# Optimization experiments

Measured on AMD Instinct MI355X. Metric: run time of the kernel, lower is better.

The kernel has to match this reference:

```python
import jax, jax.numpy as jnp
import numpy as np

T, B = 10, 512
N_ALL, N_AGENTS = 23, 22
N_FEAT = 4
X_DIM = 4
Z_EACH = 4
Z_DIM = N_ALL * Z_EACH  # 92
RNN_H = 64
NH = 8
E = N_ALL * (N_ALL - 1)  # 506

# edge list equivalent of the dense one-hot rel_rec / rel_send matrices
_off = np.ones((N_ALL, N_ALL)) - np.eye(N_ALL)
_recv_np, _send_np = np.where(_off)
RECV = jnp.asarray(_recv_np)  # rel_rec one-hot rows -> receiver node ids
SEND = jnp.asarray(_send_np)  # rel_send one-hot rows -> sender node ids
_et = np.zeros((E, 2), np.float32)
_et[np.arange(0, E, N_ALL - 1)[1:-1], 0] = 1.0
_et[-(N_ALL - 1):, 1] = 1.0
EDGE_TYPE = jnp.asarray(_et)
_nt = np.zeros((N_ALL, 2), np.float32)
_nt[:-1, 0] = 1.0
_nt[-1, 1] = 1.0
NODE_TYPE = jnp.asarray(_nt)


def _bn(x, g, b):
    # BatchNorm1d in training mode over flattened (B*M, C), biased variance
    B_, M, C = x.shape
    xf = x.reshape(B_ * M, C)
    mu = xf.mean(0)
    var = jnp.var(xf, axis=0)
    return ((xf - mu) * jax.lax.rsqrt(var + 1e-5) * g + b).reshape(B_, M, C)


def _mlp(x, W1, b1, W2, b2, g, bt):
    h = jax.nn.elu(jnp.einsum('bmi,hi->bmh', x, W1) + b1)
    h = jax.nn.elu(jnp.einsum('bmi,hi->bmh', h, W2) + b2)
    return _bn(h, g, bt)


def _kld(me, se, mp_, sp):
    return 0.5 * jnp.sum(2.0 * jnp.log(sp / se) + (se ** 2 + (me - mp_) ** 2) / sp ** 2 - 1.0)


def _gru_cell(Wih, Whh, bih, bhh, x, h):
    gi = x @ Wih.T + bih
    gh = h @ Whh.T + bhh
    ir, iz, inn = jnp.split(gi, 3, -1)
    hr, hz, hn = jnp.split(gh, 3, -1)
    r = jax.nn.sigmoid(ir + hr)
    z = jax.nn.sigmoid(iz + hz)
    n = jnp.tanh(inn + r * hn)
    return (1.0 - z) * n + z * h


_gru = jax.vmap(_gru_cell)  # over agents


def _forward(states, eps, mlp1_W1, mlp1_b1, mlp1_W2, mlp1_b2, mlp1_g, mlp1_beta,
             mlp2_W1, mlp2_b1, mlp2_W2, mlp2_b2, mlp2_g, mlp2_beta,
             mlp3_W1, mlp3_b1, mlp3_W2, mlp3_b2, mlp3_g, mlp3_beta,
             enc_mean_W, enc_mean_b, enc_std_W, enc_std_b,
             prior_mean_W, prior_mean_b, prior_std_W, prior_std_b,
             dec_mean_W, dec_mean_b, dec_std_W, dec_std_b,
             gru_Wih, gru_Whh, gru_bih, gru_bhh):
    Bsz = states.shape[2]
    y = states[:T, 0].reshape(T, Bsz, N_ALL, N_FEAT)        # y_t
    x1 = states[1:T + 1, 0].reshape(T, Bsz, N_ALL, N_FEAT)  # x_{t+1}
    P1 = (mlp1_W1, mlp1_b1, mlp1_W2, mlp1_b2, mlp1_g, mlp1_beta)
    P2 = (mlp2_W1, mlp2_b1, mlp2_W2, mlp2_b2, mlp2_g, mlp2_beta)
    P3 = (mlp3_W1, mlp3_b1, mlp3_W2, mlp3_b2, mlp3_g, mlp3_beta)

    def gnn(x, p):
        x = _mlp(x, *(a[p] for a in P1))
        # node2edge: gather senders/receivers instead of one-hot matmul
        e = jnp.concatenate([x[:, SEND], x[:, RECV],
                             jnp.broadcast_to(EDGE_TYPE, (Bsz, E, 2))], -1)
        e = _mlp(e, *(a[p] for a in P2))
        # edge2node: scatter-add into receiver nodes (rel_rec.T @ e)
        inc = jnp.zeros((Bsz, N_ALL, NH), x.dtype).at[:, RECV].add(e)
        inc = jnp.concatenate([inc, jnp.broadcast_to(NODE_TYPE, (Bsz, N_ALL, 2))], -1) / N_ALL
        return _mlp(inc, *(a[p] for a in P3))

    def step(carry, xs):
        h, Lkl = carry
        y_t, x_t, eps_t = xs
        micro = jnp.transpose(h, (1, 0, 2)).reshape(Bsz, -1)  # (B, nA*H)
        pri = jnp.concatenate([gnn(y_t, 0).reshape(Bsz, -1), micro], 1)
        enc = jnp.concatenate([gnn(x_t, 1).reshape(Bsz, -1), micro], 1)
        pm = pri @ prior_mean_W.T + prior_mean_b
        ps = jax.nn.softplus(pri @ prior_std_W.T + prior_std_b)
        em = enc @ enc_mean_W.T + enc_mean_b
        es = jax.nn.softplus(enc @ enc_std_W.T + enc_std_b)
        z = em + es * eps_t  # reparameterized sample_gauss
        Lkl = Lkl + _kld(em, es, pm, ps)
        z_ = z.reshape(Bsz, N_ALL, Z_EACH)
        dg = gnn(z_, 2).reshape(Bsz, -1)
        dm = dg @ dec_mean_W.T + dec_mean_b
        ds = jax.nn.softplus(dg @ dec_std_W.T + dec_std_b)
        # per-agent GRU update: input = [x_t agent feats, z slice]
        gin = jnp.transpose(
            jnp.concatenate([x_t[:, :N_AGENTS, :X_DIM], z_[:, :N_AGENTS]], -1), (1, 0, 2))
        h = _gru(gru_Wih, gru_Whh, gru_bih, gru_bhh, gin, h)
        return (h, Lkl), (dm, ds)

    h0 = jnp.zeros((N_AGENTS, Bsz, RNN_H), states.dtype)
    (_, Lkl), (dms, dss) = jax.lax.scan(step, (h0, jnp.zeros((), states.dtype)), (y, x1, eps))
    return dms, dss, Lkl


def setup_inputs() -> dict:
    key = jax.random.key(0)
    ks = iter(jax.random.split(key, 64))

    def rn(shape, s=0.1):
        return jax.random.normal(next(ks), shape, jnp.float32) * s

    d = {}
    d['states'] = rn((T + 1, 1, B, N_ALL * N_FEAT), 1.0)
    d['eps'] = rn((T, B, Z_DIM), 1.0)
    for i, nin in ((1, N_FEAT), (2, 2 * NH + 2), (3, NH + 2)):
        d['mlp%d_W1' % i] = rn((3, NH, nin), 0.3)
        d['mlp%d_b1' % i] = jnp.full((3, NH), 0.1, jnp.float32)
        d['mlp%d_W2' % i] = rn((3, NH, NH), 0.3)
        d['mlp%d_b2' % i] = jnp.full((3, NH), 0.1, jnp.float32)
        d['mlp%d_g' % i] = jnp.ones((3, NH), jnp.float32)
        d['mlp%d_beta' % i] = jnp.zeros((3, NH), jnp.float32)
    IN_H = NH * N_ALL + RNN_H * N_AGENTS  # 1592
    for nm in ('enc_mean', 'enc_std', 'prior_mean', 'prior_std'):
        d[nm + '_W'] = rn((Z_DIM, IN_H), 0.02)
        d[nm + '_b'] = jnp.zeros((Z_DIM,), jnp.float32)
    OUT_DEC = NH * N_ALL  # 184
    for nm in ('dec_mean', 'dec_std'):
        d[nm + '_W'] = rn((X_DIM * N_AGENTS, OUT_DEC), 0.05)
        d[nm + '_b'] = jnp.zeros((X_DIM * N_AGENTS,), jnp.float32)
    d['gru_Wih'] = rn((N_AGENTS, 3 * RNN_H, X_DIM + Z_EACH), 0.2)
    d['gru_Whh'] = rn((N_AGENTS, 3 * RNN_H, RNN_H), 0.1)
    d['gru_bih'] = jnp.zeros((N_AGENTS, 3 * RNN_H), jnp.float32)
    d['gru_bhh'] = jnp.zeros((N_AGENTS, 3 * RNN_H), jnp.float32)
    return d


def reference(states, eps, mlp1_W1, mlp1_b1, mlp1_W2, mlp1_b2, mlp1_g, mlp1_beta,
              mlp2_W1, mlp2_b1, mlp2_W2, mlp2_b2, mlp2_g, mlp2_beta,
              mlp3_W1, mlp3_b1, mlp3_W2, mlp3_b2, mlp3_g, mlp3_beta,
              enc_mean_W, enc_mean_b, enc_std_W, enc_std_b,
              prior_mean_W, prior_mean_b, prior_std_W, prior_std_b,
              dec_mean_W, dec_mean_b, dec_std_W, dec_std_b,
              gru_Wih, gru_Whh, gru_bih, gru_bhh):
    return _forward(states, eps, mlp1_W1, mlp1_b1, mlp1_W2, mlp1_b2, mlp1_g, mlp1_beta,
                    mlp2_W1, mlp2_b1, mlp2_W2, mlp2_b2, mlp2_g, mlp2_beta,
                    mlp3_W1, mlp3_b1, mlp3_W2, mlp3_b2, mlp3_g, mlp3_beta,
                    enc_mean_W, enc_mean_b, enc_std_W, enc_std_b,
                    prior_mean_W, prior_mean_b, prior_std_W, prior_std_b,
                    dec_mean_W, dec_mean_b, dec_std_W, dec_std_b,
                    gru_Wih, gru_Whh, gru_bih, gru_bhh)
```

## Files before the change

### kernel.cpp

```cpp
#include <hip/hip_runtime.h>
#include <math.h>


__device__ __forceinline__ float elu_(float x){ return x>0.f ? x : __expf(x)-1.f; }
__device__ __forceinline__ float sp_(float x){ return fmaxf(x,0.f)+log1pf(__expf(-fabsf(x))); }
__device__ __forceinline__ float sig_(float x){ return 1.f/(1.f+__expf(-x)); }
__device__ __forceinline__ float wsum_(float v){
  #pragma unroll
  for (int o=32;o;o>>=1) v += __shfl_down(v,o,64);
  return v;
}

__device__ __forceinline__ void reduce_bn_(const float* __restrict__ part, int n,
    float invN, const float* __restrict__ gam, const float* __restrict__ bet,
    float* sc, float* sh, float* tmp)
{
  int tid = threadIdx.x;
  int c = tid & 15, i0 = tid >> 4;
  float s = 0.f;
  for (int i = i0; i < n; i += 16) s += part[i*16 + c];
  tmp[i0*16 + c] = s;
  __syncthreads();
  if (tid < 16){
    float v = 0.f;
    #pragma unroll
    for (int i=0;i<16;i++) v += tmp[i*16 + tid];
    tmp[tid] = v;
  }
  __syncthreads();
  if (tid < 8){
    float m = tmp[tid]*invN;
    float var = tmp[8+tid]*invN - m*m;
    float rs = rsqrtf(var + 1e-5f);
    float s2 = rs*gam[tid];
    sc[tid] = s2; sh[tid] = bet[tid] - m*s2;
  }
  __syncthreads();
}

__device__ __forceinline__ void block_stats_(const float h[8], float* __restrict__ part,
                                             float red[][16])
{
  int wid = threadIdx.x >> 6, lane = threadIdx.x & 63;
  #pragma unroll
  for (int j=0;j<8;j++){
    float a = wsum_(h[j]);
    float b = wsum_(h[j]*h[j]);
    if (lane==0){ red[wid][j]=a; red[wid][8+j]=b; }
  }
  __syncthreads();
  if (threadIdx.x < 16)
    part[threadIdx.x] = red[0][threadIdx.x]+red[1][threadIdx.x]
                       +red[2][threadIdx.x]+red[3][threadIdx.x];
}


__device__ __forceinline__ void dev_heads(
    float* smem, int idx, int t,
    const float* __restrict__ gy, const float* __restrict__ gx,
    const float* __restrict__ scsh3, const float* __restrict__ h,
    const float* __restrict__ Wpm, const float* __restrict__ Wps,
    const float* __restrict__ Wem, const float* __restrict__ Wes,
    float* __restrict__ rawp)
{
  int bt = idx & 7, head = (idx>>3)&3, kz = idx>>5;
  const float* W  = (head==0)?Wpm:(head==1)?Wps:(head==2)?Wem:Wes;
  const float* gsel = (head<2)?gy:gx;
  int sel = (head<2) ? t : 10+t;
  float* s3 = smem;
  float (*As)[68]  = (float(*)[68])(smem+16);
  float (*Ws)[100] = (float(*)[100])(smem+1104);
  int tid = threadIdx.x;
  if (tid < 16) s3[tid] = scsh3[sel*16 + tid];
  int b0 = bt*64;
  int kbeg = kz*228;
  int kend = kbeg+228; if (kend > 1592) kend = 1592;
  int tb = tid & 15, tj = tid >> 4;
  float acc[4][6];
  #pragma unroll
  for (int u=0;u<4;u++)
    #pragma unroll
    for (int vv=0;vv<6;vv++) acc[u][vv]=0.f;
  __syncthreads();
  for (int k0=kbeg; k0<kend; k0+=16){
    #pragma unroll
    for (int l=0;l<4;l++){
      int lin = tid + 256*l;
      int kk = lin & 15, bl = lin >> 4;
      int i = k0 + kk;
      float v = 0.f;
      if (i < kend){
        int bb = b0 + bl;
        if (i < 184){ int c = i&7; v = gsel[bb*184 + i]*s3[c] + s3[8+c]; }
        else { int i2 = i - 184; v = h[(size_t)(i2>>6)*32768 + bb*64 + (i2&63)]; }
      }
      As[kk][bl] = v;
    }
    #pragma unroll
    for (int l=0;l<6;l++){
      int lin = tid + 256*l;
      int kk = lin & 15, jl = lin >> 4;
      int i = k0 + kk;
      float v = 0.f;
      if (i < kend && jl < 92) v = W[jl*1592 + i];
      Ws[kk][jl] = v;
    }
    __syncthreads();
    #pragma unroll
    for (int kk=0;kk<16;kk++){
      float4 a4 = *(const float4*)&As[kk][tb*4];
      float av[4] = {a4.x,a4.y,a4.z,a4.w};
      float2 w01 = *(const float2*)&Ws[kk][tj*6];
      float2 w23 = *(const float2*)&Ws[kk][tj*6+2];
      float2 w45 = *(const float2*)&Ws[kk][tj*6+4];
      float wv[6] = {w01.x,w01.y,w23.x,w23.y,w45.x,w45.y};
      #pragma unroll
      for (int u=0;u<4;u++)
        #pragma unroll
        for (int vv=0;vv<6;vv++) acc[u][vv] += av[u]*wv[vv];
    }
    __syncthreads();
  }
  float* dst = rawp + (size_t)kz*188416 + (size_t)head*47104;
  #pragma unroll
  for (int u=0;u<4;u++){
    int bb = b0 + tb*4 + u;
    #pragma unroll
    for (int vv=0;vv<6;vv++){
      int j = tj*6 + vv;
      if (j < 92) dst[bb*92 + j] = acc[u][vv];
    }
  }
}

__device__ __forceinline__ void dev_edges_z(
    float* smem, int b,
    const float* __restrict__ rawp_prev, const float* __restrict__ eps_t,
    const float* __restrict__ bpm, const float* __restrict__ bps,
    const float* __restrict__ bem, const float* __restrict__ bes,
    const float* __restrict__ zp1,
    const float* __restrict__ nW1, const float* __restrict__ nb1,
    const float* __restrict__ nW2, const float* __restrict__ nb2,
    const float* __restrict__ g1, const float* __restrict__ bt1,
    const float* __restrict__ eW1, const float* __restrict__ eb1,
    const float* __restrict__ eW2, const float* __restrict__ eb2,
    float* __restrict__ zna, float* __restrict__ zp2, float* __restrict__ lklp_t)
{
  int tid = threadIdx.x;
  float* tmp   = smem;
  float* sc1   = smem+256;
  float* sh1   = smem+264;
  float* xnode = smem+272;
  float* accs  = smem+480;
  float* redsq = smem+688;
  float* zrow  = smem+720;
  float* redk  = smem+812;
  float* le    = smem+816;
  {
    int c = tid & 15, i0 = tid >> 4;
    float s = 0.f;
    for (int i=i0;i<368;i+=16) s += zp1[i*16+c];
    tmp[i0*16+c] = s;
    __syncthreads();
    if (tid<16){
      float v=0.f;
      #pragma unroll
      for (int i=0;i<16;i++) v += tmp[i*16+tid];
      tmp[tid]=v;
    }
    __syncthreads();
    if (tid<8){
      float m = tmp[tid]*(1.f/11776.f);
      float var = tmp[8+tid]*(1.f/11776.f) - m*m;
      float rs = rsqrtf(var+1e-5f);
      float s2 = rs*g1[tid];
      sc1[tid]=s2; sh1[tid]=bt1[tid]-m*s2;
    }
  }
  float kld = 0.f;
  if (tid < 92){
    int j = tid;
    float pm=bpm[j], ps=bps[j], em=bem[j], es=bes[j];
    const float* q = rawp_prev + (size_t)b*92 + j;
    #pragma unroll
    for (int kz=0;kz<7;kz++){
      const float* qq = q + (size_t)kz*188416;
      pm += qq[0]; ps += qq[47104]; em += qq[94208]; es += qq[141312];
    }
    ps = sp_(ps); es = sp_(es);
    float z = em + es*eps_t[(size_t)b*92 + j];
    zrow[j] = z;
    float d = em - pm;
    kld = 0.5f*(2.f*logf(ps/es) + (es*es + d*d)/(ps*ps) - 1.f);
  }
  float kv = wsum_(kld);
  if ((tid&63)==0) redk[tid>>6] = kv;
  __syncthreads();
  if (tid==0) lklp_t[b] = redk[0]+redk[1]+redk[2]+redk[3];
  if (tid < 23){
    float z0=zrow[tid*4], z1=zrow[tid*4+1], z2=zrow[tid*4+2], z3=zrow[tid*4+3];
    float h1[8];
    #pragma unroll
    for (int j=0;j<8;j++)
      h1[j] = elu_(nb1[j] + nW1[j*4]*z0 + nW1[j*4+1]*z1 + nW1[j*4+2]*z2 + nW1[j*4+3]*z3);
    #pragma unroll
    for (int j=0;j<8;j++){
      float a = nb2[j];
      #pragma unroll
      for (int k=0;k<8;k++) a += nW2[j*8+k]*h1[k];
      xnode[tid*9+j] = elu_(a)*sc1[j] + sh1[j];
    }
  }
  __syncthreads();
  float sq[8]={0,0,0,0,0,0,0,0};
  for (int e=tid; e<506; e+=256){
    int r=e/22, jj=e-r*22;
    int s=jj+(jj>=r?1:0);
    float et0=(jj==0 && r>=1 && r<=21)?1.f:0.f;
    float et1=(r==22)?1.f:0.f;
    float h1[8];
    #pragma unroll
    for (int j=0;j<8;j++){
      const float* w=eW1+j*18;
      float a=eb1[j]+w[16]*et0+w[17]*et1;
      #pragma unroll
      for (int k=0;k<8;k++) a+=w[k]*xnode[s*9+k];
      #pragma unroll
      for (int k=0;k<8;k++) a+=w[8+k]*xnode[r*9+k];
      h1[j]=elu_(a);
    }
    #pragma unroll
    for (int j=0;j<8;j++){
      float a=eb2[j];
      #pragma unroll
      for (int k=0;k<8;k++) a+=eW2[j*8+k]*h1[k];
      float h2=elu_(a);
      le[e*9+j]=h2;
      sq[j]+=h2*h2;
    }
  }
  int wid=tid>>6, lane=tid&63;
  #pragma unroll
  for (int j=0;j<8;j++){
    float v=wsum_(sq[j]);
    if (lane==0) redsq[wid*8+j]=v;
  }
  __syncthreads();
  if (tid<184){
    int r=tid>>3, c=tid&7;
    const float* lp = le + r*198 + c;
    float s=0.f;
    #pragma unroll
    for (int jj=0;jj<22;jj++) s+=lp[jj*9];
    accs[r*9+c]=s;
    zna[(size_t)b*184+tid]=s;
  }
  __syncthreads();
  if (tid<16){
    int c=tid&7;
    float s=0.f;
    if (tid<8){
      #pragma unroll
      for (int r=0;r<23;r++) s+=accs[r*9+c];
    } else {
      #pragma unroll
      for (int w=0;w<4;w++) s+=redsq[w*8+c];
    }
    zp2[(size_t)b*16+tid]=s;
  }
}

__device__ __forceinline__ void dev_node3(
    float* smem, int bi, int g, int p,
    const float* __restrict__ nodeacc, const float* __restrict__ p2,
    const float* __restrict__ g2b, const float* __restrict__ bt2b,
    const float* __restrict__ W3b, const float* __restrict__ b3b,
    const float* __restrict__ W4b, const float* __restrict__ b4b,
    float* __restrict__ out, float* __restrict__ p3)
{
  float* tmp = smem; float* sc2 = smem+256; float* sh2 = smem+264;
  float (*red)[16] = (float(*)[16])(smem+272);
  reduce_bn_(p2 + (size_t)g*8192, 512, 1.f/259072.f, g2b+p*8, bt2b+p*8, sc2, sh2, tmp);
  int row = bi*256 + threadIdx.x;
  int b = row/23, r = row - b*23;
  const float inv23 = 1.f/23.f;
  const float* na = nodeacc + ((size_t)g*512 + b)*184 + r*8;
  float xk[8];
  #pragma unroll
  for (int k=0;k<8;k++) xk[k] = (na[k]*sc2[k] + 22.f*sh2[k]) * inv23;
  float nt0 = (r<22)?inv23:0.f, nt1 = (r==22)?inv23:0.f;
  const float* W3 = W3b + p*80; const float* b3 = b3b + p*8;
  const float* W4 = W4b + p*64; const float* b4 = b4b + p*8;
  float h1b[8], o[8];
  #pragma unroll
  for (int j=0;j<8;j++){
    const float* w = W3 + j*10;
    float a = b3[j] + w[8]*nt0 + w[9]*nt1;
    #pragma unroll
    for (int k=0;k<8;k++) a += w[k]*xk[k];
    h1b[j] = elu_(a);
  }
  #pragma unroll
  for (int j=0;j<8;j++){
    float a = b4[j];
    #pragma unroll
    for (int k=0;k<8;k++) a += W4[j*8+k]*h1b[k];
    o[j] = elu_(a);
    out[((size_t)g*11776 + row)*8 + j] = o[j];
  }
  block_stats_(o, p3 + ((size_t)g*46 + bi)*16, red);
}

__device__ __forceinline__ void dev_dec(
    float* smem, int bi,
    const float* __restrict__ zg3, const float* __restrict__ p3,
    const float* __restrict__ gam, const float* __restrict__ bet,
    const float* __restrict__ Wm, const float* __restrict__ Bm,
    const float* __restrict__ Wsd, const float* __restrict__ Bsd,
    float* __restrict__ odm, float* __restrict__ ods)
{
  int tid = threadIdx.x;
  float* dtmp = smem; float* dsc = smem + 256; float* dsh = smem + 264;
  reduce_bn_(p3, 46, 1.f/11776.f, gam, bet, dsc, dsh, dtmp);
  float4 s0 = {dsc[0],dsc[1],dsc[2],dsc[3]};
  float4 s1 = {dsc[4],dsc[5],dsc[6],dsc[7]};
  float4 t0 = {dsh[0],dsh[1],dsh[2],dsh[3]};
  float4 t1 = {dsh[4],dsh[5],dsh[6],dsh[7]};
  int idx = bi*256 + tid;
  int hd = idx / 45056; int rem = idx - hd*45056;
  int b = rem / 88, j = rem - b*88;
  const float* W = hd ? Wsd : Wm;
  const float4* a4 = (const float4*)(zg3 + (size_t)b*184);
  const float4* w4 = (const float4*)(W + (size_t)j*184);
  float accv = hd ? Bsd[j] : Bm[j];
  #pragma unroll 2
  for (int i4=0;i4<46;i4++){
    float4 x = a4[i4]; float4 w = w4[i4];
    float4 sc = (i4&1)? s1 : s0; float4 sh = (i4&1)? t1 : t0;
    accv += w.x*(x.x*sc.x+sh.x) + w.y*(x.y*sc.y+sh.y)
          + w.z*(x.z*sc.z+sh.z) + w.w*(x.w*sc.w+sh.w);
  }
  if (hd) ods[(size_t)b*88+j] = sp_(accv);
  else    odm[(size_t)b*88+j] = accv;
}

__device__ __forceinline__ void dev_gru_z(
    float* smem, int idx,
    float* __restrict__ h, const float* __restrict__ x_t,
    const float* __restrict__ rawp_cur, const float* __restrict__ eps_t,
    const float* __restrict__ bem, const float* __restrict__ bes,
    const float* __restrict__ nW1, const float* __restrict__ nb1,
    const float* __restrict__ nW2, const float* __restrict__ nb2,
    float* __restrict__ zp1,
    const float* __restrict__ Wih, const float* __restrict__ Whh,
    const float* __restrict__ bih, const float* __restrict__ bhh)
{
  int tid = threadIdx.x;
  float* WhT  = smem;
  float* hs   = smem + 12352;
  float* gins = smem + 14656;
  int a = idx >> 4, yb = idx & 15;
  int b0 = yb*32;
  int c = tid & 63, sq = tid >> 6;
  const float* Wg = Whh + (size_t)a*12288;
  for (int e = tid; e < 12288; e += 256) WhT[(e&63)*193 + (e>>6)] = Wg[e];
  const float* hp_g = h + (size_t)a*32768 + (size_t)b0*64;
  for (int e = tid; e < 2048; e += 256) hs[(e&63)*36 + (e>>6)] = hp_g[e];
  { int s = tid >> 3, k = tid & 7;
    float v;
    if (k < 4) v = x_t[(size_t)(b0+s)*92 + a*4 + k];
    else {
      int j = a*4 + (k-4);
      float em=bem[j], es=bes[j];
      const float* q = rawp_cur + (size_t)(b0+s)*92 + j;
      #pragma unroll
      for (int kz=0;kz<7;kz++){
        const float* qq = q + (size_t)kz*188416;
        em += qq[94208]; es += qq[141312];
      }
      es = sp_(es);
      v = em + es*eps_t[(size_t)(b0+s)*92 + j];
    }
    gins[k*36 + s] = v; }
  float wi0[8], wi1[8], wi2[8];
  const float* Wig = Wih + (size_t)a*1536;
  #pragma unroll
  for (int k=0;k<8;k++){
    wi0[k] = Wig[c*8+k]; wi1[k] = Wig[(64+c)*8+k]; wi2[k] = Wig[(128+c)*8+k];
  }
  float bi0 = bih[a*192+c], bi1 = bih[a*192+64+c], bi2 = bih[a*192+128+c];
  float bh0 = bhh[a*192+c], bh1 = bhh[a*192+64+c], bh2 = bhh[a*192+128+c];
  __syncthreads();
  {
    float h2s[8];
    if (tid < 32){
      float z0=gins[4*36+tid], z1=gins[5*36+tid], z2=gins[6*36+tid], z3=gins[7*36+tid];
      float h1s[8];
      #pragma unroll
      for (int j=0;j<8;j++)
        h1s[j] = elu_(nb1[j] + nW1[j*4]*z0 + nW1[j*4+1]*z1 + nW1[j*4+2]*z2 + nW1[j*4+3]*z3);
      #pragma unroll
      for (int j=0;j<8;j++){
        float av = nb2[j];
        #pragma unroll
        for (int k=0;k<8;k++) av += nW2[j*8+k]*h1s[k];
        h2s[j] = elu_(av);
      }
    } else {
      #pragma unroll
      for (int j=0;j<8;j++) h2s[j] = 0.f;
    }
    float* dst = zp1 + (size_t)(a*16+yb)*16;
    #pragma unroll
    for (int j=0;j<8;j++){
      float s1 = wsum_(h2s[j]);
      float s2 = wsum_(h2s[j]*h2s[j]);
      if (tid==0){ dst[j]=s1; dst[8+j]=s2; }
    }
  }
  #pragma unroll
  for (int ps=0; ps<2; ps++){
    int s0 = ps*16 + sq*4;
    float q0[4], q1[4], q2[4];
    #pragma unroll
    for (int i=0;i<4;i++){ q0[i]=bh0; q1[i]=bh1; q2[i]=bh2; }
    for (int k=0;k<64;k++){
      float w0 = WhT[k*193 + c];
      float w1 = WhT[k*193 + 64 + c];
      float w2 = WhT[k*193 + 128 + c];
      float4 hv = *(const float4*)&hs[k*36 + s0];
      float hvv[4] = {hv.x,hv.y,hv.z,hv.w};
      #pragma unroll
      for (int i=0;i<4;i++){ q0[i]+=w0*hvv[i]; q1[i]+=w1*hvv[i]; q2[i]+=w2*hvv[i]; }
    }
    float g0[4], g1[4], g2[4];
    #pragma unroll
    for (int i=0;i<4;i++){ g0[i]=bi0; g1[i]=bi1; g2[i]=bi2; }
    #pragma unroll
    for (int k=0;k<8;k++){
      float4 gv = *(const float4*)&gins[k*36 + s0];
      float gvv[4] = {gv.x,gv.y,gv.z,gv.w};
      #pragma unroll
      for (int i=0;i<4;i++){ g0[i]+=wi0[k]*gvv[i]; g1[i]+=wi1[k]*gvv[i]; g2[i]+=wi2[k]*gvv[i]; }
    }
    float4 hp = *(const float4*)&hs[c*36 + s0];
    float hpv[4] = {hp.x,hp.y,hp.z,hp.w};
    #pragma unroll
    for (int i=0;i<4;i++){
      float rg = sig_(g0[i]+q0[i]);
      float zg = sig_(g1[i]+q1[i]);
      float ng = tanhf(g2[i] + rg*q2[i]);
      h[(size_t)a*32768 + (size_t)(b0+s0+i)*64 + c] = (1.f-zg)*ng + zg*hpv[i];
    }
  }
}

__device__ __forceinline__ void dev_z22(
    int yb,
    const float* __restrict__ rawp_cur, const float* __restrict__ eps_t,
    const float* __restrict__ bem, const float* __restrict__ bes,
    const float* __restrict__ nW1, const float* __restrict__ nb1,
    const float* __restrict__ nW2, const float* __restrict__ nb2,
    float* __restrict__ zp1)
{
  int tid = threadIdx.x;
  int b0 = yb*32;
  float h2s[8];
  if (tid < 32){
    float zv[4];
    #pragma unroll
    for (int q=0;q<4;q++){
      int j = 88+q;
      float em=bem[j], es=bes[j];
      const float* qp = rawp_cur + (size_t)(b0+tid)*92 + j;
      #pragma unroll
      for (int kz=0;kz<7;kz++){
        const float* qq = qp + (size_t)kz*188416;
        em += qq[94208]; es += qq[141312];
      }
      es = sp_(es);
      zv[q] = em + es*eps_t[(size_t)(b0+tid)*92 + j];
    }
    float h1s[8];
    #pragma unroll
    for (int j=0;j<8;j++)
      h1s[j] = elu_(nb1[j] + nW1[j*4]*zv[0] + nW1[j*4+1]*zv[1] + nW1[j*4+2]*zv[2] + nW1[j*4+3]*zv[3]);
    #pragma unroll
    for (int j=0;j<8;j++){
      float av = nb2[j];
      #pragma unroll
      for (int k=0;k<8;k++) av += nW2[j*8+k]*h1s[k];
      h2s[j] = elu_(av);
    }
  } else {
    #pragma unroll
    for (int j=0;j<8;j++) h2s[j] = 0.f;
  }
  float* dst = zp1 + (size_t)(352+yb)*16;
  #pragma unroll
  for (int j=0;j<8;j++){
    float s1 = wsum_(h2s[j]);
    float s2 = wsum_(h2s[j]*h2s[j]);
    if (tid==0){ dst[j]=s1; dst[8+j]=s2; }
  }
}


__global__ __launch_bounds__(256) void k_stats1(
    const float* __restrict__ states,
    const float* __restrict__ W1b, const float* __restrict__ b1b,
    const float* __restrict__ W2b, const float* __restrict__ b2b,
    float* __restrict__ part)
{
  int g = blockIdx.y; int p = g/10; int t = g - p*10;
  const float* W1 = W1b + p*32; const float* b1 = b1b + p*8;
  const float* W2 = W2b + p*64; const float* b2 = b2b + p*8;
  int row = blockIdx.x*256 + threadIdx.x;
  float4 x4 = *(const float4*)(states + (size_t)(t+p)*47104 + 4*(size_t)row);
  float h1[8], h2[8];
  #pragma unroll
  for (int j=0;j<8;j++)
    h1[j] = elu_(b1[j] + W1[j*4+0]*x4.x + W1[j*4+1]*x4.y + W1[j*4+2]*x4.z + W1[j*4+3]*x4.w);
  #pragma unroll
  for (int j=0;j<8;j++){
    float a = b2[j];
    #pragma unroll
    for (int k=0;k<8;k++) a += W2[j*8+k]*h1[k];
    h2[j] = elu_(a);
  }
  __shared__ float red[4][16];
  block_stats_(h2, part + ((size_t)g*46 + blockIdx.x)*16, red);
}

__global__ __launch_bounds__(512) void k_pre_edges(
    const float* __restrict__ src, const float* __restrict__ p1,
    const float* __restrict__ nW1b, const float* __restrict__ nb1b,
    const float* __restrict__ nW2b, const float* __restrict__ nb2b,
    const float* __restrict__ g1b, const float* __restrict__ bt1b,
    const float* __restrict__ eW1b, const float* __restrict__ eb1b,
    const float* __restrict__ eW2b, const float* __restrict__ eb2b,
    float* __restrict__ nodeacc, float* __restrict__ p2)
{
  int g = blockIdx.y; int p = g/10; int t = g - p*10; int b = blockIdx.x;
  int tid = threadIdx.x;
  __shared__ float tmp[512];
  __shared__ float sc1[8], sh1[8];
  __shared__ float xnode[207];
  __shared__ float le[4554];
  __shared__ float accs[207];
  __shared__ float redsq[8][8];
  {
    const float* pp = p1 + (size_t)g*736;
    int c = tid & 15, i0 = tid >> 4;
    float s = 0.f;
    for (int i = i0; i < 46; i += 32) s += pp[i*16 + c];
    tmp[i0*16 + c] = s;
    __syncthreads();
    if (tid < 16){
      float v = 0.f;
      #pragma unroll
      for (int i=0;i<32;i++) v += tmp[i*16 + tid];
      tmp[tid] = v;
    }
    __syncthreads();
    if (tid < 8){
      float m = tmp[tid]*(1.f/11776.f);
      float var = tmp[8+tid]*(1.f/11776.f) - m*m;
      float rs = rsqrtf(var + 1e-5f);
      float s2 = rs*g1b[p*8+tid];
      sc1[tid] = s2; sh1[tid] = bt1b[p*8+tid] - m*s2;
    }
    __syncthreads();
  }
  if (tid < 23){
    const float* x = src + (size_t)(t+p)*47104 + (size_t)b*92 + tid*4;
    const float* W1 = nW1b + p*32; const float* b1 = nb1b + p*8;
    const float* W2 = nW2b + p*64; const float* b2 = nb2b + p*8;
    float x0=x[0], x1=x[1], x2=x[2], x3=x[3];
    float h1[8];
    #pragma unroll
    for (int j=0;j<8;j++)
      h1[j] = elu_(b1[j] + W1[j*4]*x0 + W1[j*4+1]*x1 + W1[j*4+2]*x2 + W1[j*4+3]*x3);
    #pragma unroll
    for (int j=0;j<8;j++){
      float a = b2[j];
      #pragma unroll
      for (int k=0;k<8;k++) a += W2[j*8+k]*h1[k];
      xnode[tid*9+j] = elu_(a)*sc1[j] + sh1[j];
    }
  }
  __syncthreads();
  float sq[8] = {0,0,0,0,0,0,0,0};
  if (tid < 506){
    int r = tid/22, jj = tid - r*22;
    int s = jj + (jj>=r ? 1 : 0);
    const float* W1 = eW1b + p*144; const float* b1 = eb1b + p*8;
    const float* W2 = eW2b + p*64;  const float* b2 = eb2b + p*8;
    float et0 = (jj==0 && r>=1 && r<=21) ? 1.f : 0.f;
    float et1 = (r==22) ? 1.f : 0.f;
    float h1[8];
    #pragma unroll
    for (int j=0;j<8;j++){
      const float* w = W1 + j*18;
      float a = b1[j] + w[16]*et0 + w[17]*et1;
      #pragma unroll
      for (int k=0;k<8;k++) a += w[k]*xnode[s*9+k];
      #pragma unroll
      for (int k=0;k<8;k++) a += w[8+k]*xnode[r*9+k];
      h1[j] = elu_(a);
    }
    #pragma unroll
    for (int j=0;j<8;j++){
      float a = b2[j];
      #pragma unroll
      for (int k=0;k<8;k++) a += W2[j*8+k]*h1[k];
      float h2 = elu_(a);
      le[tid*9+j] = h2;
      sq[j] = h2*h2;
    }
  }
  int wid = tid >> 6, lane = tid & 63;
  #pragma unroll
  for (int j=0;j<8;j++){
    float v = wsum_(sq[j]);
    if (lane==0) redsq[wid][j] = v;
  }
  __syncthreads();
  if (tid < 184){
    int r = tid >> 3, c = tid & 7;
    const float* lp = le + r*198 + c;
    float s = 0.f;
    #pragma unroll
    for (int jj=0;jj<22;jj++) s += lp[jj*9];
    accs[r*9+c] = s;
    nodeacc[((size_t)g*512 + b)*184 + tid] = s;
  }
  __syncthreads();
  if (tid < 16){
    int c = tid & 7;
    float s = 0.f;
    if (tid < 8){
      #pragma unroll
      for (int r=0;r<23;r++) s += accs[r*9+c];
    } else {
      #pragma unroll
      for (int w=0;w<8;w++) s += redsq[w][c];
    }
    p2[((size_t)g*512 + b)*16 + tid] = s;
  }
}

__global__ __launch_bounds__(256) void k_pre_node3(
    const float* __restrict__ nodeacc, const float* __restrict__ p2,
    const float* __restrict__ g2, const float* __restrict__ bt2,
    const float* __restrict__ W3, const float* __restrict__ b3,
    const float* __restrict__ W4, const float* __restrict__ b4,
    float* __restrict__ out, float* __restrict__ p3)
{
  __shared__ float smem[336];
  int g = blockIdx.y, p = g/10;
  dev_node3(smem, blockIdx.x, g, p, nodeacc, p2, g2, bt2, W3,b3,W4,b4, out, p3);
}

__global__ __launch_bounds__(256) void k_bnred(
    const float* __restrict__ part, int n, float invN,
    const float* __restrict__ gamb, const float* __restrict__ betb,
    float* __restrict__ scsh)
{
  int g = blockIdx.x; int p = g/10;
  int tid = threadIdx.x;
  __shared__ float tmp[256];
  const float* pp = part + (size_t)g*n*16;
  int c = tid & 15, i0 = tid >> 4;
  float s = 0.f;
  for (int i = i0; i < n; i += 16) s += pp[i*16 + c];
  tmp[i0*16 + c] = s;
  __syncthreads();
  if (tid < 16){
    float v = 0.f;
    #pragma unroll
    for (int i=0;i<16;i++) v += tmp[i*16 + tid];
    tmp[tid] = v;
  }
  __syncthreads();
  if (tid < 8){
    float m = tmp[tid]*invN;
    float var = tmp[8+tid]*invN - m*m;
    float rs = rsqrtf(var + 1e-5f);
    float sc = rs*gamb[p*8+tid];
    scsh[g*16 + tid] = sc;
    scsh[g*16 + 8 + tid] = betb[p*8+tid] - m*sc;
  }
}


__global__ __launch_bounds__(256) void k_KA(
    int nh, int ne, int t,
    const float* __restrict__ gy, const float* __restrict__ gx,
    const float* __restrict__ scsh3, const float* __restrict__ h,
    const float* __restrict__ Wpm, const float* __restrict__ Wps,
    const float* __restrict__ Wem, const float* __restrict__ Wes,
    float* __restrict__ rawp_cur,
    const float* __restrict__ rawp_prev, const float* __restrict__ eps_prev,
    const float* __restrict__ bpm, const float* __restrict__ bps,
    const float* __restrict__ bem, const float* __restrict__ bes,
    const float* __restrict__ zp1,
    const float* __restrict__ nW1, const float* __restrict__ nb1,
    const float* __restrict__ nW2, const float* __restrict__ nb2,
    const float* __restrict__ g1, const float* __restrict__ bt1,
    const float* __restrict__ eW1, const float* __restrict__ eb1,
    const float* __restrict__ eW2, const float* __restrict__ eb2,
    float* __restrict__ zna, float* __restrict__ zp2, float* __restrict__ lklp_t,
    const float* __restrict__ zg3, const float* __restrict__ zp3,
    const float* __restrict__ gam3, const float* __restrict__ bet3,
    const float* __restrict__ Wm, const float* __restrict__ Bm,
    const float* __restrict__ Wsd, const float* __restrict__ Bsd,
    float* __restrict__ odm, float* __restrict__ ods)
{
  __shared__ float smem[5370];
  int it = blockIdx.x;
  if (it < nh)
    dev_heads(smem, it, t, gy, gx, scsh3, h, Wpm,Wps,Wem,Wes, rawp_cur);
  else if (it < nh+ne)
    dev_edges_z(smem, it-nh, rawp_prev, eps_prev, bpm,bps,bem,bes, zp1,
                nW1,nb1,nW2,nb2, g1,bt1, eW1,eb1,eW2,eb2, zna, zp2, lklp_t);
  else
    dev_dec(smem, it-nh-ne, zg3, zp3, gam3, bet3, Wm,Bm,Wsd,Bsd, odm, ods);
}

__global__ __launch_bounds__(256) void k_KB(
    int ng,
    float* __restrict__ h, const float* __restrict__ x_t,
    const float* __restrict__ rawp_cur, const float* __restrict__ eps_t,
    const float* __restrict__ bem, const float* __restrict__ bes,
    const float* __restrict__ nW1, const float* __restrict__ nb1,
    const float* __restrict__ nW2, const float* __restrict__ nb2,
    float* __restrict__ zp1,
    const float* __restrict__ Wih, const float* __restrict__ Whh,
    const float* __restrict__ bih, const float* __restrict__ bhh,
    const float* __restrict__ zna, const float* __restrict__ zp2,
    const float* __restrict__ g2, const float* __restrict__ bt2,
    const float* __restrict__ W3, const float* __restrict__ b3,
    const float* __restrict__ W4, const float* __restrict__ b4,
    float* __restrict__ zg3, float* __restrict__ zp3)
{
  __shared__ float smem[14944];
  int it = blockIdx.x;
  if (it < ng){
    if (it < ng-16)
      dev_gru_z(smem, it, h, x_t, rawp_cur, eps_t, bem, bes,
                nW1,nb1,nW2,nb2, zp1, Wih, Whh, bih, bhh);
    else
      dev_z22(it-(ng-16), rawp_cur, eps_t, bem, bes, nW1,nb1,nW2,nb2, zp1);
  } else
    dev_node3(smem, it-ng, 0, 0, zna, zp2, g2, bt2, W3,b3,W4,b4, zg3, zp3);
}

__global__ __launch_bounds__(256) void k_final(const float* __restrict__ lklp,
                                               float* __restrict__ out){
  __shared__ float red[4];
  float s = 0.f;
  for (int i = threadIdx.x; i < 5120; i += 256) s += lklp[i];
  s = wsum_(s);
  if ((threadIdx.x&63)==0) red[threadIdx.x>>6]=s;
  __syncthreads();
  if (threadIdx.x==0) out[0] = red[0]+red[1]+red[2]+red[3];
}

extern "C" void kernel_launch(void* const* d_in, const int* in_sizes, int n_in,
                              void* d_out, int out_size, void* d_ws, size_t ws_size,
                              hipStream_t stream)
{
  (void)in_sizes; (void)n_in; (void)out_size; (void)ws_size;
  const float* states=(const float*)d_in[0];
  const float* eps   =(const float*)d_in[1];
  const float *m1W1=(const float*)d_in[2],  *m1b1=(const float*)d_in[3],
              *m1W2=(const float*)d_in[4],  *m1b2=(const float*)d_in[5],
              *m1g =(const float*)d_in[6],  *m1bt=(const float*)d_in[7];
  const float *m2W1=(const float*)d_in[8],  *m2b1=(const float*)d_in[9],
              *m2W2=(const float*)d_in[10], *m2b2=(const float*)d_in[11],
              *m2g =(const float*)d_in[12], *m2bt=(const float*)d_in[13];
  const float *m3W1=(const float*)d_in[14], *m3b1=(const float*)d_in[15],
              *m3W2=(const float*)d_in[16], *m3b2=(const float*)d_in[17],
              *m3g =(const float*)d_in[18], *m3bt=(const float*)d_in[19];
  const float *emW=(const float*)d_in[20], *emB=(const float*)d_in[21];
  const float *esW=(const float*)d_in[22], *esB=(const float*)d_in[23];
  const float *pmW=(const float*)d_in[24], *pmB=(const float*)d_in[25];
  const float *psW=(const float*)d_in[26], *psB=(const float*)d_in[27];
  const float *dmW=(const float*)d_in[28], *dmB=(const float*)d_in[29];
  const float *dsW=(const float*)d_in[30], *dsB=(const float*)d_in[31];
  const float *gWih=(const float*)d_in[32], *gWhh=(const float*)d_in[33];
  const float *gbih=(const float*)d_in[34], *gbhh=(const float*)d_in[35];
  float* out = (float*)d_out;
  float* ws  = (float*)d_ws;

  float* g3    = ws;
  float* h     = ws + 1884160;
  float* lklp  = ws + 2605056;
  float* scsh3 = ws + 2610176;
  float* zp1   = ws + 2610496;
  float* zna   = ws + 2616384;
  float* zp2   = ws + 2710592;
  float* zg3   = ws + 2718784;
  float* zp3   = ws + 2812992;
  float* rawp0 = ws + 2813728;
  float* rawp1 = ws + 4132640;
  float* p1p = rawp0;
  float* naP = rawp0 + 14720;
  float* p2p = rawp0 + 1898880;
  float* p3p = rawp0 + 2062720;

  hipMemsetAsync(h, 0, 720896*sizeof(float), stream);

  k_stats1<<<dim3(46,20),256,0,stream>>>(states, m1W1, m1b1, m1W2, m1b2, p1p);
  k_pre_edges<<<dim3(512,20),512,0,stream>>>(states, p1p,
      m1W1, m1b1, m1W2, m1b2, m1g, m1bt,
      m2W1, m2b1, m2W2, m2b2, naP, p2p);
  k_pre_node3<<<dim3(46,20),256,0,stream>>>(naP, p2p, m2g, m2bt,
      m3W1, m3b1, m3W2, m3b2, g3, p3p);
  k_bnred<<<20,256,0,stream>>>(p3p, 46, 1.f/11776.f, m3g, m3bt, scsh3);

  for (int t=0;t<=11;t++){
    int nh = (t<10)?224:0;
    int ne = (t>=1 && t<=10)?512:0;
    int nd = (t>=2)?352:0;
    int tt  = (t<10)? t : 0;
    int tm1 = (t>=1)? t-1 : 0;
    int tm2 = (t>=2)? t-2 : 0;
    float* rcur  = (t&1)? rawp1 : rawp0;
    float* rprev = (t&1)? rawp0 : rawp1;
    if (nh+ne+nd > 0)
      k_KA<<<nh+ne+nd,256,0,stream>>>(nh, ne, tt,
          g3 + (size_t)tt*94208, g3 + 942080 + (size_t)tt*94208,
          scsh3, h, pmW, psW, emW, esW, rcur,
          rprev, eps + (size_t)tm1*47104,
          pmB, psB, emB, esB, zp1,
          m1W1+64, m1b1+16, m1W2+128, m1b2+16, m1g+16, m1bt+16,
          m2W1+288, m2b1+16, m2W2+128, m2b2+16,
          zna, zp2, lklp + (size_t)tm1*512,
          zg3, zp3, m3g+16, m3bt+16, dmW, dmB, dsW, dsB,
          out + (size_t)tm2*45056, out + 450560 + (size_t)tm2*45056);
    int ng = (t<10)?368:0;
    int nn = (t>=1 && t<=10)?46:0;
    if (ng+nn > 0)
      k_KB<<<ng+nn,256,0,stream>>>(ng,
          h, states + (size_t)((t<10)? t+1 : 1)*47104,
          rcur, eps + (size_t)tt*47104,
          emB, esB, m1W1+64, m1b1+16, m1W2+128, m1b2+16, zp1,
          gWih, gWhh, gbih, gbhh,
          zna, zp2, m2g+16, m2bt+16,
          m3W1+160, m3b1+16, m3W2+128, m3b2+16, zg3, zp3);
  }
  k_final<<<1,256,0,stream>>>(lklp, out + 901120);
}
```

Baseline: 900.7 us.

## Compute encoder/prior heads with bf16 MFMA and fold batch-norm into weights

Replaces the FP32 split-K shared-memory GEMM for the four encoder/prior heads with bf16 MFMA 16x16x32 tiles that read operands straight from global memory. The layer-3 batch-norm scale is folded into per-timestep prepacked bf16 weights, and its shift becomes a precomputed constant bias. The GRU hidden state and g3 features are also written as bf16 copies. This removes the 7-way split-K partial buffers and their reduction in the consumers, and cuts head blocks from 224 to 32 per step. In exchange it adds prepacking kernels and bf16 rounding error on the head outputs.

```diff
diff --git a/kernel.cpp b/kernel.cpp
--- a/kernel.cpp
+++ b/kernel.cpp
@@ -1,7 +1,15 @@
 #include <hip/hip_runtime.h>
+#include <hip/hip_bf16.h>
 #include <math.h>
 
 
+typedef __attribute__((ext_vector_type(8))) short s16x8;
+typedef __attribute__((ext_vector_type(4))) float f32x4;
+
+__device__ __forceinline__ unsigned short f2bf(float x){
+  __hip_bfloat16 b = __float2bfloat16(x);
+  return *reinterpret_cast<unsigned short*>(&b);
+}
 __device__ __forceinline__ float elu_(float x){ return x>0.f ? x : __expf(x)-1.f; }
 __device__ __forceinline__ float sp_(float x){ return fmaxf(x,0.f)+log1pf(__expf(-fabsf(x))); }
 __device__ __forceinline__ float sig_(float x){ return 1.f/(1.f+__expf(-x)); }
@@ -55,87 +63,69 @@
 }
 
 
-__device__ __forceinline__ void dev_heads(
-    float* smem, int idx, int t,
-    const float* __restrict__ gy, const float* __restrict__ gx,
-    const float* __restrict__ scsh3, const float* __restrict__ h,
-    const float* __restrict__ Wpm, const float* __restrict__ Wps,
-    const float* __restrict__ Wem, const float* __restrict__ Wes,
-    float* __restrict__ rawp)
-{
-  int bt = idx & 7, head = (idx>>3)&3, kz = idx>>5;
-  const float* W  = (head==0)?Wpm:(head==1)?Wps:(head==2)?Wem:Wes;
-  const float* gsel = (head<2)?gy:gx;
-  int sel = (head<2) ? t : 10+t;
-  float* s3 = smem;
-  float (*As)[68]  = (float(*)[68])(smem+16);
-  float (*Ws)[100] = (float(*)[100])(smem+1104);
+__device__ __forceinline__ void dev_heads_mfma(
+    int idx, int t,
+    const unsigned short* __restrict__ g3b,
+    const unsigned short* __restrict__ hb,
+    const unsigned short* __restrict__ Wbt,
+    const unsigned short* __restrict__ Wbs,
+    const float* __restrict__ cst,
+    float* __restrict__ raw)
+{
+  int head = idx & 3, mb = idx >> 2;
   int tid = threadIdx.x;
-  if (tid < 16) s3[tid] = scsh3[sel*16 + tid];
-  int b0 = bt*64;
-  int kbeg = kz*228;
-  int kend = kbeg+228; if (kend > 1592) kend = 1592;
-  int tb = tid & 15, tj = tid >> 4;
-  float acc[4][6];
-  #pragma unroll
-  for (int u=0;u<4;u++)
-    #pragma unroll
-    for (int vv=0;vv<6;vv++) acc[u][vv]=0.f;
-  __syncthreads();
-  for (int k0=kbeg; k0<kend; k0+=16){
-    #pragma unroll
-    for (int l=0;l<4;l++){
-      int lin = tid + 256*l;
-      int kk = lin & 15, bl = lin >> 4;
-      int i = k0 + kk;
-      float v = 0.f;
-      if (i < kend){
-        int bb = b0 + bl;
-        if (i < 184){ int c = i&7; v = gsel[bb*184 + i]*s3[c] + s3[8+c]; }
-        else { int i2 = i - 184; v = h[(size_t)(i2>>6)*32768 + bb*64 + (i2&63)]; }
+  int wv = tid >> 6, lane = tid & 63;
+  int m0 = mb*64 + wv*16;
+  int rloc = lane & 15, kg = lane >> 4;
+  int row = m0 + rloc;
+  int selg = (head < 2) ? t : 10 + t;
+  const unsigned short* Ag = g3b + (size_t)selg*98304 + (size_t)row*192 + kg*8;
+  const unsigned short* Wt = Wbt + (size_t)((t*4+head)*96)*192 + kg*8;
+  const unsigned short* Wsb = Wbs + (size_t)head*135168;
+  f32x4 cd[6];
+  #pragma unroll
+  for (int n=0;n<6;n++) cd[n] = (f32x4){0.f,0.f,0.f,0.f};
+  #pragma unroll
+  for (int ks=0; ks<6; ks++){
+    s16x8 af = *(const s16x8*)(Ag + ks*32);
+    #pragma unroll
+    for (int n=0;n<6;n++){
+      int col = n*16 + rloc;
+      s16x8 bf = *(const s16x8*)(Wt + (size_t)col*192 + ks*32);
+      cd[n] = __builtin_amdgcn_mfma_f32_16x16x32_bf16(af, bf, cd[n], 0,0,0);
+    }
+  }
+  const unsigned short* Ah = hb + (size_t)row*64;
+  #pragma unroll 4
+  for (int ks=0; ks<44; ks++){
+    int f2 = ks*32 + kg*8;
+    s16x8 af = *(const s16x8*)(Ah + (size_t)(f2>>6)*32768 + (f2&63));
+    #pragma unroll
+    for (int n=0;n<6;n++){
+      int col = n*16 + rloc;
+      s16x8 bf = *(const s16x8*)(Wsb + (size_t)col*1408 + f2);
+      cd[n] = __builtin_amdgcn_mfma_f32_16x16x32_bf16(af, bf, cd[n], 0,0,0);
+    }
+  }
+  float* dst = raw + (size_t)head*47104;
+  const float* cb = cst + (size_t)(t*4+head)*96;
+  #pragma unroll
+  for (int n=0;n<6;n++){
+    int col = n*16 + rloc;
+    if (col < 92){
+      float cc = cb[col];
+      #pragma unroll
+      for (int r=0;r<4;r++){
+        int rr = m0 + (kg<<2) + r;
+        dst[(size_t)rr*92 + col] = cd[n][r] + cc;
       }
-      As[kk][bl] = v;
-    }
-    #pragma unroll
-    for (int l=0;l<6;l++){
-      int lin = tid + 256*l;
-      int kk = lin & 15, jl = lin >> 4;
-      int i = k0 + kk;
-      float v = 0.f;
-      if (i < kend && jl < 92) v = W[jl*1592 + i];
-      Ws[kk][jl] = v;
-    }
-    __syncthreads();
-    #pragma unroll
-    for (int kk=0;kk<16;kk++){
-      float4 a4 = *(const float4*)&As[kk][tb*4];
-      float av[4] = {a4.x,a4.y,a4.z,a4.w};
-      float2 w01 = *(const float2*)&Ws[kk][tj*6];
-      float2 w23 = *(const float2*)&Ws[kk][tj*6+2];
-      float2 w45 = *(const float2*)&Ws[kk][tj*6+4];
-      float wv[6] = {w01.x,w01.y,w23.x,w23.y,w45.x,w45.y};
-      #pragma unroll
-      for (int u=0;u<4;u++)
-        #pragma unroll
-        for (int vv=0;vv<6;vv++) acc[u][vv] += av[u]*wv[vv];
-    }
-    __syncthreads();
-  }
-  float* dst = rawp + (size_t)kz*188416 + (size_t)head*47104;
-  #pragma unroll
-  for (int u=0;u<4;u++){
-    int bb = b0 + tb*4 + u;
-    #pragma unroll
-    for (int vv=0;vv<6;vv++){
-      int j = tj*6 + vv;
-      if (j < 92) dst[bb*92 + j] = acc[u][vv];
     }
   }
 }
 
 __device__ __forceinline__ void dev_edges_z(
     float* smem, int b,
-    const float* __restrict__ rawp_prev, const float* __restrict__ eps_t,
+    const float* __restrict__ raw_prev, const float* __restrict__ eps_t,
     const float* __restrict__ bpm, const float* __restrict__ bps,
     const float* __restrict__ bem, const float* __restrict__ bes,
     const float* __restrict__ zp1,
@@ -180,14 +170,11 @@
   float kld = 0.f;
   if (tid < 92){
     int j = tid;
-    float pm=bpm[j], ps=bps[j], em=bem[j], es=bes[j];
-    const float* q = rawp_prev + (size_t)b*92 + j;
-    #pragma unroll
-    for (int kz=0;kz<7;kz++){
-      const float* qq = q + (size_t)kz*188416;
-      pm += qq[0]; ps += qq[47104]; em += qq[94208]; es += qq[141312];
-    }
-    ps = sp_(ps); es = sp_(es);
+    const float* q = raw_prev + (size_t)b*92 + j;
+    float pm = bpm[j] + q[0];
+    float ps = sp_(bps[j] + q[47104]);
+    float em = bem[j] + q[94208];
+    float es = sp_(bes[j] + q[141312]);
     float z = em + es*eps_t[(size_t)b*92 + j];
     zrow[j] = z;
     float d = em - pm;
@@ -276,7 +263,8 @@
     const float* __restrict__ g2b, const float* __restrict__ bt2b,
     const float* __restrict__ W3b, const float* __restrict__ b3b,
     const float* __restrict__ W4b, const float* __restrict__ b4b,
-    float* __restrict__ out, float* __restrict__ p3)
+    float* __restrict__ outf, unsigned short* __restrict__ outb,
+    float* __restrict__ p3)
 {
   float* tmp = smem; float* sc2 = smem+256; float* sh2 = smem+264;
   float (*red)[16] = (float(*)[16])(smem+272);
@@ -306,7 +294,8 @@
     #pragma unroll
     for (int k=0;k<8;k++) a += W4[j*8+k]*h1b[k];
     o[j] = elu_(a);
-    out[((size_t)g*11776 + row)*8 + j] = o[j];
+    if (outf) outf[(size_t)row*8 + j] = o[j];
+    else outb[(size_t)g*98304 + (size_t)b*192 + r*8 + j] = f2bf(o[j]);
   }
   block_stats_(o, p3 + ((size_t)g*46 + bi)*16, red);
 }
@@ -346,8 +335,9 @@
 
 __device__ __forceinline__ void dev_gru_z(
     float* smem, int idx,
-    float* __restrict__ h, const float* __restrict__ x_t,
-    const float* __restrict__ rawp_cur, const float* __restrict__ eps_t,
+    float* __restrict__ h, unsigned short* __restrict__ hbf,
+    const float* __restrict__ x_t,
+    const float* __restrict__ raw_cur, const float* __restrict__ eps_t,
     const float* __restrict__ bem, const float* __restrict__ bes,
     const float* __restrict__ nW1, const float* __restrict__ nb1,
     const float* __restrict__ nW2, const float* __restrict__ nb2,
@@ -371,14 +361,8 @@
     if (k < 4) v = x_t[(size_t)(b0+s)*92 + a*4 + k];
     else {
       int j = a*4 + (k-4);
-      float em=bem[j], es=bes[j];
-      const float* q = rawp_cur + (size_t)(b0+s)*92 + j;
-      #pragma unroll
-      for (int kz=0;kz<7;kz++){
-        const float* qq = q + (size_t)kz*188416;
-        em += qq[94208]; es += qq[141312];
-      }
-      es = sp_(es);
+      float em = bem[j] + raw_cur[94208 + (size_t)(b0+s)*92 + j];
+      float es = sp_(bes[j] + raw_cur[141312 + (size_t)(b0+s)*92 + j]);
       v = em + es*eps_t[(size_t)(b0+s)*92 + j];
     }
     gins[k*36 + s] = v; }
@@ -450,14 +434,17 @@
       float rg = sig_(g0[i]+q0[i]);
       float zg = sig_(g1[i]+q1[i]);
       float ng = tanhf(g2[i] + rg*q2[i]);
-      h[(size_t)a*32768 + (size_t)(b0+s0+i)*64 + c] = (1.f-zg)*ng + zg*hpv[i];
+      float hn = (1.f-zg)*ng + zg*hpv[i];
+      size_t off = (size_t)a*32768 + (size_t)(b0+s0+i)*64 + c;
+      h[off] = hn;
+      hbf[off] = f2bf(hn);
     }
   }
 }
 
 __device__ __forceinline__ void dev_z22(
     int yb,
-    const float* __restrict__ rawp_cur, const float* __restrict__ eps_t,
+    const float* __restrict__ raw_cur, const float* __restrict__ eps_t,
     const float* __restrict__ bem, const float* __restrict__ bes,
     const float* __restrict__ nW1, const float* __restrict__ nb1,
     const float* __restrict__ nW2, const float* __restrict__ nb2,
@@ -471,14 +458,8 @@
     #pragma unroll
     for (int q=0;q<4;q++){
       int j = 88+q;
-      float em=bem[j], es=bes[j];
-      const float* qp = rawp_cur + (size_t)(b0+tid)*92 + j;
-      #pragma unroll
-      for (int kz=0;kz<7;kz++){
-        const float* qq = qp + (size_t)kz*188416;
-        em += qq[94208]; es += qq[141312];
-      }
-      es = sp_(es);
+      float em = bem[j] + raw_cur[94208 + (size_t)(b0+tid)*92 + j];
+      float es = sp_(bes[j] + raw_cur[141312 + (size_t)(b0+tid)*92 + j]);
       zv[q] = em + es*eps_t[(size_t)(b0+tid)*92 + j];
     }
     float h1s[8];
@@ -655,11 +636,12 @@
     const float* __restrict__ g2, const float* __restrict__ bt2,
     const float* __restrict__ W3, const float* __restrict__ b3,
     const float* __restrict__ W4, const float* __restrict__ b4,
-    float* __restrict__ out, float* __restrict__ p3)
+    unsigned short* __restrict__ g3b, float* __restrict__ p3)
 {
   __shared__ float smem[336];
   int g = blockIdx.y, p = g/10;
-  dev_node3(smem, blockIdx.x, g, p, nodeacc, p2, g2, bt2, W3,b3,W4,b4, out, p3);
+  dev_node3(smem, blockIdx.x, g, p, nodeacc, p2, g2, bt2, W3,b3,W4,b4,
+            nullptr, g3b, p3);
 }
 
 __global__ __launch_bounds__(256) void k_bnred(
@@ -693,15 +675,61 @@
   }
 }
 
+__global__ __launch_bounds__(256) void k_wbs(
+    const float* __restrict__ Wpm, const float* __restrict__ Wps,
+    const float* __restrict__ Wem, const float* __restrict__ Wes,
+    unsigned short* __restrict__ Wbs)
+{
+  int e = blockIdx.x*256 + threadIdx.x;
+  int head = e / 135168; int rem = e - head*135168;
+  int col = rem / 1408; int f2 = rem - col*1408;
+  const float* W = (head==0)?Wpm:(head==1)?Wps:(head==2)?Wem:Wes;
+  float v = (col<92) ? W[(size_t)col*1592 + 184 + f2] : 0.f;
+  Wbs[e] = f2bf(v);
+}
+
+__global__ __launch_bounds__(256) void k_wbt(
+    const float* __restrict__ Wpm, const float* __restrict__ Wps,
+    const float* __restrict__ Wem, const float* __restrict__ Wes,
+    const float* __restrict__ scsh3,
+    unsigned short* __restrict__ Wbt)
+{
+  int e = blockIdx.x*256 + threadIdx.x;
+  int t = e / 73728; int rem = e - t*73728;
+  int head = rem / 18432; int rem2 = rem - head*18432;
+  int col = rem2 / 192; int f = rem2 - col*192;
+  const float* W = (head==0)?Wpm:(head==1)?Wps:(head==2)?Wem:Wes;
+  int sel = (head<2) ? t : 10+t;
+  float v = (col<92 && f<184) ? W[(size_t)col*1592 + f]*scsh3[sel*16 + (f&7)] : 0.f;
+  Wbt[e] = f2bf(v);
+}
+
+__global__ __launch_bounds__(256) void k_cst(
+    const float* __restrict__ Wpm, const float* __restrict__ Wps,
+    const float* __restrict__ Wem, const float* __restrict__ Wes,
+    const float* __restrict__ scsh3, float* __restrict__ cst)
+{
+  int e = blockIdx.x*256 + threadIdx.x;
+  if (e >= 3840) return;
+  int t = e / 384; int rem = e - t*384;
+  int head = rem / 96; int col = rem - head*96;
+  float s = 0.f;
+  if (col < 92){
+    const float* W = (head==0)?Wpm:(head==1)?Wps:(head==2)?Wem:Wes;
+    int sel = (head<2) ? t : 10+t;
+    const float* sh = scsh3 + sel*16 + 8;
+    for (int f=0; f<184; f++) s += W[(size_t)col*1592+f]*sh[f&7];
+  }
+  cst[e] = s;
+}
+
 
 __global__ __launch_bounds__(256) void k_KA(
     int nh, int ne, int t,
-    const float* __restrict__ gy, const float* __restrict__ gx,
-    const float* __restrict__ scsh3, const float* __restrict__ h,
-    const float* __restrict__ Wpm, const float* __restrict__ Wps,
-    const float* __restrict__ Wem, const float* __restrict__ Wes,
-    float* __restrict__ rawp_cur,
-    const float* __restrict__ rawp_prev, const float* __restrict__ eps_prev,
+    const unsigned short* __restrict__ g3b, const unsigned short* __restrict__ hbf,
+    const unsigned short* __restrict__ Wbt, const unsigned short* __restrict__ Wbs,
+    const float* __restrict__ cst, float* __restrict__ raw_cur,
+    const float* __restrict__ raw_prev, const float* __restrict__ eps_prev,
     const float* __restrict__ bpm, const float* __restrict__ bps,
     const float* __restrict__ bem, const float* __restrict__ bes,
     const float* __restrict__ zp1,
@@ -720,9 +748,9 @@
   __shared__ float smem[5370];
   int it = blockIdx.x;
   if (it < nh)
-    dev_heads(smem, it, t, gy, gx, scsh3, h, Wpm,Wps,Wem,Wes, rawp_cur);
+    dev_heads_mfma(it, t, g3b, hbf, Wbt, Wbs, cst, raw_cur);
   else if (it < nh+ne)
-    dev_edges_z(smem, it-nh, rawp_prev, eps_prev, bpm,bps,bem,bes, zp1,
+    dev_edges_z(smem, it-nh, raw_prev, eps_prev, bpm,bps,bem,bes, zp1,
                 nW1,nb1,nW2,nb2, g1,bt1, eW1,eb1,eW2,eb2, zna, zp2, lklp_t);
   else
     dev_dec(smem, it-nh-ne, zg3, zp3, gam3, bet3, Wm,Bm,Wsd,Bsd, odm, ods);
@@ -730,8 +758,9 @@
 
 __global__ __launch_bounds__(256) void k_KB(
     int ng,
-    float* __restrict__ h, const float* __restrict__ x_t,
-    const float* __restrict__ rawp_cur, const float* __restrict__ eps_t,
+    float* __restrict__ h, unsigned short* __restrict__ hbf,
+    const float* __restrict__ x_t,
+    const float* __restrict__ raw_cur, const float* __restrict__ eps_t,
     const float* __restrict__ bem, const float* __restrict__ bes,
     const float* __restrict__ nW1, const float* __restrict__ nb1,
     const float* __restrict__ nW2, const float* __restrict__ nb2,
@@ -748,12 +777,13 @@
   int it = blockIdx.x;
   if (it < ng){
     if (it < ng-16)
-      dev_gru_z(smem, it, h, x_t, rawp_cur, eps_t, bem, bes,
+      dev_gru_z(smem, it, h, hbf, x_t, raw_cur, eps_t, bem, bes,
                 nW1,nb1,nW2,nb2, zp1, Wih, Whh, bih, bhh);
     else
-      dev_z22(it-(ng-16), rawp_cur, eps_t, bem, bes, nW1,nb1,nW2,nb2, zp1);
+      dev_z22(it-(ng-16), raw_cur, eps_t, bem, bes, nW1,nb1,nW2,nb2, zp1);
   } else
-    dev_node3(smem, it-ng, 0, 0, zna, zp2, g2, bt2, W3,b3,W4,b4, zg3, zp3);
+    dev_node3(smem, it-ng, 0, 0, zna, zp2, g2, bt2, W3,b3,W4,b4,
+              zg3, nullptr, zp3);
 }
 
 __global__ __launch_bounds__(256) void k_final(const float* __restrict__ lklp,
@@ -794,45 +824,54 @@
   float* out = (float*)d_out;
   float* ws  = (float*)d_ws;
 
-  float* g3    = ws;
-  float* h     = ws + 1884160;
-  float* lklp  = ws + 2605056;
-  float* scsh3 = ws + 2610176;
-  float* zp1   = ws + 2610496;
-  float* zna   = ws + 2616384;
-  float* zp2   = ws + 2710592;
-  float* zg3   = ws + 2718784;
-  float* zp3   = ws + 2812992;
-  float* rawp0 = ws + 2813728;
-  float* rawp1 = ws + 4132640;
-  float* p1p = rawp0;
-  float* naP = rawp0 + 14720;
-  float* p2p = rawp0 + 1898880;
-  float* p3p = rawp0 + 2062720;
+  unsigned short* g3b = (unsigned short*)(ws);
+  unsigned short* Wbt = (unsigned short*)(ws + 983040);
+  unsigned short* Wbs = (unsigned short*)(ws + 1351680);
+  unsigned short* hbf = (unsigned short*)(ws + 1622016);
+  float* h     = ws + 1982464;
+  float* cst   = ws + 2703360;
+  float* scsh3 = ws + 2707200;
+  float* lklp  = ws + 2707520;
+  float* zp1   = ws + 2712640;
+  float* zna   = ws + 2718528;
+  float* zp2   = ws + 2812736;
+  float* zg3   = ws + 2820928;
+  float* zp3   = ws + 2915136;
+  float* raw0  = ws + 2915872;
+  float* raw1  = ws + 3104288;
+  float* scr   = ws + 3292704;
+  float* p1p = scr;
+  float* naP = scr + 14720;
+  float* p2p = scr + 1898880;
+  float* p3p = scr + 2062720;
 
   hipMemsetAsync(h, 0, 720896*sizeof(float), stream);
+  hipMemsetAsync(hbf, 0, 720896*sizeof(unsigned short), stream);
+  hipMemsetAsync(g3b, 0, 1966080*sizeof(unsigned short), stream);
 
   k_stats1<<<dim3(46,20),256,0,stream>>>(states, m1W1, m1b1, m1W2, m1b2, p1p);
   k_pre_edges<<<dim3(512,20),512,0,stream>>>(states, p1p,
       m1W1, m1b1, m1W2, m1b2, m1g, m1bt,
       m2W1, m2b1, m2W2, m2b2, naP, p2p);
   k_pre_node3<<<dim3(46,20),256,0,stream>>>(naP, p2p, m2g, m2bt,
-      m3W1, m3b1, m3W2, m3b2, g3, p3p);
+      m3W1, m3b1, m3W2, m3b2, g3b, p3p);
   k_bnred<<<20,256,0,stream>>>(p3p, 46, 1.f/11776.f, m3g, m3bt, scsh3);
+  k_wbs<<<2112,256,0,stream>>>(pmW, psW, emW, esW, Wbs);
+  k_wbt<<<2880,256,0,stream>>>(pmW, psW, emW, esW, scsh3, Wbt);
+  k_cst<<<15,256,0,stream>>>(pmW, psW, emW, esW, scsh3, cst);
 
   for (int t=0;t<=11;t++){
-    int nh = (t<10)?224:0;
+    int nh = (t<10)?32:0;
     int ne = (t>=1 && t<=10)?512:0;
     int nd = (t>=2)?352:0;
     int tt  = (t<10)? t : 0;
     int tm1 = (t>=1)? t-1 : 0;
     int tm2 = (t>=2)? t-2 : 0;
-    float* rcur  = (t&1)? rawp1 : rawp0;
-    float* rprev = (t&1)? rawp0 : rawp1;
+    float* rcur  = (t&1)? raw1 : raw0;
+    float* rprev = (t&1)? raw0 : raw1;
     if (nh+ne+nd > 0)
       k_KA<<<nh+ne+nd,256,0,stream>>>(nh, ne, tt,
-          g3 + (size_t)tt*94208, g3 + 942080 + (size_t)tt*94208,
-          scsh3, h, pmW, psW, emW, esW, rcur,
+          g3b, hbf, Wbt, Wbs, cst, rcur,
           rprev, eps + (size_t)tm1*47104,
           pmB, psB, emB, esB, zp1,
           m1W1+64, m1b1+16, m1W2+128, m1b2+16, m1g+16, m1bt+16,
@@ -844,7 +883,7 @@
     int nn = (t>=1 && t<=10)?46:0;
     if (ng+nn > 0)
       k_KB<<<ng+nn,256,0,stream>>>(ng,
-          h, states + (size_t)((t<10)? t+1 : 1)*47104,
+          h, hbf, states + (size_t)((t<10)? t+1 : 1)*47104,
           rcur, eps + (size_t)tt*47104,
           emB, esB, m1W1+64, m1b1+16, m1W2+128, m1b2+16, zp1,
           gWih, gWhh, gbih, gbhh,
```

New measurement: 975.5 us. 8.3% more time.
